# Kernel tuning notes

Hardware: AMD Instinct MI355X
Metric: run time of the kernel (lower is better)

The kernel has to match this reference:

```python
import jax, jax.numpy as jnp
import numpy as np

HIDDEN = 2048
N_HEADS = 32
N_KV = 8
HEAD_DIM = 128
EPS = 1e-6
THETA = 10000.0
WINDOW = 512
T = 2048


def _rms_norm(x, w, eps=EPS):
    # x: [..., d]
    var = jnp.mean(x * x, axis=-1, keepdims=True)
    return x * jax.lax.rsqrt(var + eps) * w


def _rope(x, positions):
    # neox-style full rotary, x: [T, H, d]
    d = x.shape[-1]
    inv_freq = 1.0 / (THETA ** (jnp.arange(0, d, 2, dtype=jnp.float32) / d))  # [d/2]
    ang = positions.astype(jnp.float32)[:, None] * inv_freq  # [T, d/2]
    cos = jnp.cos(ang)[:, None, :]  # [T,1,d/2]
    sin = jnp.sin(ang)[:, None, :]
    x1, x2 = x[..., : d // 2], x[..., d // 2 :]
    return jnp.concatenate([x1 * cos - x2 * sin, x2 * cos + x1 * sin], axis=-1)


def setup_inputs() -> dict:
    key = jax.random.key(0)
    ks = jax.random.split(key, 6)
    q_size = N_HEADS * HEAD_DIM
    kv_size = N_KV * HEAD_DIM
    s = 1.0 / np.sqrt(HIDDEN)
    return {
        "positions": jnp.arange(T, dtype=jnp.int32),
        "hidden_states": jax.random.normal(ks[0], (T, HIDDEN), dtype=jnp.float32),
        "w_qkv": jax.random.normal(ks[1], (HIDDEN, q_size + 2 * kv_size), dtype=jnp.float32) * s,
        "w_o": jax.random.normal(ks[2], (q_size, HIDDEN), dtype=jnp.float32) * s,
        "w_g": jax.random.normal(ks[3], (HIDDEN, N_HEADS), dtype=jnp.float32) * s,
        "q_norm_w": jnp.ones((HEAD_DIM,), dtype=jnp.float32),
        "k_norm_w": jnp.ones((HEAD_DIM,), dtype=jnp.float32),
    }


def reference(positions, hidden_states, w_qkv, w_o, w_g, q_norm_w, k_norm_w):
    t = hidden_states.shape[0]
    q_size = N_HEADS * HEAD_DIM
    kv_size = N_KV * HEAD_DIM
    scale = HEAD_DIM ** -0.5
    group = N_HEADS // N_KV

    qkv = hidden_states @ w_qkv  # [T, q+2kv]
    q = qkv[:, :q_size].reshape(t, N_HEADS, HEAD_DIM)
    k = qkv[:, q_size : q_size + kv_size].reshape(t, N_KV, HEAD_DIM)
    v = qkv[:, q_size + kv_size :].reshape(t, N_KV, HEAD_DIM)

    # per-head RMSNorm then RoPE
    q = _rope(_rms_norm(q, q_norm_w), positions)
    k = _rope(_rms_norm(k, k_norm_w), positions)

    # sliding-window causal attention with GQA (group queries per kv head)
    qg = q.reshape(t, N_KV, group, HEAD_DIM)
    scores = jnp.einsum("tkgd,skd->kgts", qg, k) * scale  # [Hkv,G,T,T]
    diff = positions[:, None] - positions[None, :]  # i - j
    mask = (diff >= 0) & (diff < WINDOW)  # causal + sliding window
    scores = jnp.where(mask[None, None], scores, -jnp.inf)
    probs = jax.nn.softmax(scores, axis=-1)
    attn = jnp.einsum("kgts,skd->tkgd", probs, v).reshape(t, N_HEADS, HEAD_DIM)

    # softplus gate per head, then output projection
    gate = jax.nn.softplus((hidden_states @ w_g).astype(jnp.float32)).astype(attn.dtype)
    attn = attn * gate[:, :, None]
    return attn.reshape(t, q_size) @ w_o
```

## Files before the change

### kernel.cpp

```cpp
#include <hip/hip_runtime.h>

typedef __attribute__((ext_vector_type(4))) float floatx4;
typedef __attribute__((ext_vector_type(8))) _Float16 half8;
typedef __attribute__((ext_vector_type(4))) _Float16 half4;

#define TT 2048
#define HIDDEN 2048
#define NH 32
#define NKV 8
#define HD 128
#define QSIZE 4096
#define KVSIZE 1024
#define QKVN 6144
#define QKVNP 6272
#define VOFF 5120
#define GOFF 6144
#define WINDOW 512

__global__ __launch_bounds__(256) void prep_kernel(
    const float* __restrict__ w_qkv, const float* __restrict__ w_o,
    const float* __restrict__ hidden, const float* __restrict__ w_g,
    _Float16* __restrict__ Wqkvt, _Float16* __restrict__ Wot,
    _Float16* __restrict__ Xb) {
  __shared__ float tile[64][68];
  int bid = blockIdx.x;
  int tid = threadIdx.x;
  if (bid >= 5120) {
    if (bid < 7168) {
      int i = ((bid - 5120) * 256 + tid) * 8;
      float4 a = *(const float4*)&hidden[i];
      float4 b = *(const float4*)&hidden[i + 4];
      alignas(16) _Float16 o[8] = {(_Float16)a.x, (_Float16)a.y, (_Float16)a.z, (_Float16)a.w,
                                   (_Float16)b.x, (_Float16)b.y, (_Float16)b.z, (_Float16)b.w};
      *(uint4*)&Xb[i] = *(const uint4*)o;
    } else if (bid < 7264) {
      int i = ((bid - 7168) * 256 + tid) * 8;
      *(uint4*)&Wqkvt[(size_t)(GOFF + NH) * HIDDEN + i] = (uint4){0, 0, 0, 0};
    } else {
      int br = (bid - 7264) * 32;
      int c = tid & 31, r0 = tid >> 5;
      __shared__ float gt[32][33];
#pragma unroll
      for (int i = 0; i < 4; ++i) {
        int r = r0 + 8 * i;
        gt[r][c] = w_g[(size_t)(br + r) * NH + c];
      }
      __syncthreads();
#pragma unroll
      for (int i = 0; i < 4; ++i) {
        int r = r0 + 8 * i;
        Wqkvt[(size_t)(GOFF + r) * HIDDEN + br + c] = (_Float16)gt[c][r];
      }
    }
    return;
  }
  const float* in;
  _Float16* out;
  int R, C, tilesX, t;
  if (bid < 3072) { in = w_qkv; out = Wqkvt; R = HIDDEN; C = QKVN; tilesX = 96; t = bid; }
  else           { in = w_o;   out = Wot;   R = QSIZE;  C = HIDDEN; tilesX = 32; t = bid - 3072; }
  int bc = (t % tilesX) * 64, br = (t / tilesX) * 64;
  int rr = tid >> 4, l16 = tid & 15;
#pragma unroll
  for (int it = 0; it < 4; ++it) {
    int r = rr + it * 16;
    *(float4*)&tile[r][l16 * 4] = *(const float4*)&in[(size_t)(br + r) * C + bc + l16 * 4];
  }
  __syncthreads();
  int orow = tid >> 2, rr0 = (tid & 3) * 16;
  alignas(16) _Float16 tmp[16];
#pragma unroll
  for (int jj = 0; jj < 16; ++jj) tmp[jj] = (_Float16)tile[rr0 + jj][orow];
  *(uint4*)&out[(size_t)(bc + orow) * R + br + rr0] = *(const uint4*)&tmp[0];
  *(uint4*)&out[(size_t)(bc + orow) * R + br + rr0 + 8] = *(const uint4*)&tmp[8];
}

__global__ __launch_bounds__(256) void repack_kv_kernel(const _Float16* __restrict__ Kh,
                                                        const _Float16* __restrict__ QKVh,
                                                        _Float16* __restrict__ Kf,
                                                        _Float16* __restrict__ Vf) {
  __shared__ _Float16 tile[64][136];
  int st = blockIdx.x, kh = blockIdx.y;
  int s0 = st * 64;
  if (blockIdx.z == 0) {
    _Float16* dst = Kf + (size_t)(kh * 32 + st) * 8192;
#pragma unroll
    for (int i = 0; i < 4; ++i) {
      int c = threadIdx.x + i * 256;
      int jt = c >> 8, kc = (c >> 6) & 3, quad = (c >> 4) & 3, n16 = c & 15;
      uint4 v = *(const uint4*)&Kh[((size_t)(s0 + jt * 16 + n16) * NKV + kh) * HD +
                                   kc * 32 + quad * 8];
      *(uint4*)&dst[c * 8] = v;
    }
  } else {
#pragma unroll
    for (int i = 0; i < 4; ++i) {
      int c = threadIdx.x + i * 256;
      int row = c >> 4, part = c & 15;
      *(uint4*)&tile[row][part * 8] =
          *(const uint4*)&QKVh[(size_t)(s0 + row) * QKVNP + VOFF + kh * HD + part * 8];
    }
    __syncthreads();
    _Float16* dst = Vf + (size_t)(kh * 32 + st) * 8192;
#pragma unroll
    for (int i = 0; i < 4; ++i) {
      int c = threadIdx.x + i * 256;
      int jd = c >> 7, kc = (c >> 6) & 1, quad = (c >> 4) & 3, n16 = c & 15;
      int d = jd * 16 + n16, sb = kc * 32 + quad * 8;
      alignas(16) _Float16 tmp[8];
#pragma unroll
      for (int j = 0; j < 8; ++j) tmp[j] = tile[sb + j][d];
      *(uint4*)&dst[c * 8] = *(const uint4*)tmp;
    }
  }
}

__device__ __forceinline__ void async16(const _Float16* g, _Float16* l) {
  __builtin_amdgcn_global_load_lds((const __attribute__((address_space(1))) void*)g,
                                   (__attribute__((address_space(3))) void*)l, 16, 0, 0);
}

__device__ __forceinline__ void swizzle_mn(int& m0, int& n0) {
  int ntiles = gridDim.y;
  int pid = blockIdx.x + blockIdx.y * gridDim.x;
  int band = pid / (8 * ntiles);
  int wi = pid - band * (8 * ntiles);
  m0 = (band * 8 + (wi & 7)) * 128;
  n0 = (wi >> 3) * 128;
}

template <typename OutT>
__global__ __launch_bounds__(256, 2) void gemm_bt_kernel(
    const _Float16* __restrict__ A, const _Float16* __restrict__ Bt,
    OutT* __restrict__ C, int M, int N, int K) {
  __shared__ _Float16 As[128 * 64];
  __shared__ _Float16 Bs[128 * 64];
  int tid = threadIdx.x;
  int wave = tid >> 6, lane = tid & 63;
  int wm = wave >> 1, wn = wave & 1;
  int m0, n0;
  swizzle_mn(m0, n0);
  int lr = lane & 15;
  int quad = lane >> 4;
  floatx4 acc[4][4];
#pragma unroll
  for (int i = 0; i < 4; ++i)
#pragma unroll
    for (int j = 0; j < 4; ++j) acc[i][j] = (floatx4){0.f, 0.f, 0.f, 0.f};

  for (int k0 = 0; k0 < K; k0 += 64) {
    __syncthreads();
#pragma unroll
    for (int it = 0; it < 4; ++it) {
      int c = tid + it * 256;
      int row = c >> 3, j = c & 7;
      int jj = j ^ (row & 7);
      _Float16* la = &As[it * 2048 + wave * 512];
      _Float16* lb = &Bs[it * 2048 + wave * 512];
      async16(&A[(size_t)(m0 + row) * K + k0 + jj * 8], la);
      async16(&Bt[(size_t)(n0 + row) * K + k0 + jj * 8], lb);
    }
    __syncthreads();
#pragma unroll
    for (int kc = 0; kc < 2; ++kc) {
      int ch = kc * 4 + quad;
      half8 a[4], b[4];
#pragma unroll
      for (int i = 0; i < 4; ++i) {
        int r = wm * 64 + i * 16 + lr;
        a[i] = *(const half8*)&As[r * 64 + (ch ^ (r & 7)) * 8];
      }
#pragma unroll
      for (int j = 0; j < 4; ++j) {
        int r = wn * 64 + j * 16 + lr;
        b[j] = *(const half8*)&Bs[r * 64 + (ch ^ (r & 7)) * 8];
      }
#pragma unroll
      for (int i = 0; i < 4; ++i)
#pragma unroll
        for (int j = 0; j < 4; ++j)
          acc[i][j] = __builtin_amdgcn_mfma_f32_16x16x32_f16(a[i], b[j], acc[i][j], 0, 0, 0);
    }
  }
  int rq = quad * 4;
#pragma unroll
  for (int i = 0; i < 4; ++i)
#pragma unroll
    for (int j = 0; j < 4; ++j)
#pragma unroll
      for (int r = 0; r < 4; ++r) {
        int row = m0 + wm * 64 + i * 16 + rq + r;
        int col = n0 + wn * 64 + j * 16 + lr;
        C[(size_t)row * N + col] = (OutT)acc[i][j][r];
      }
}

__global__ __launch_bounds__(256, 2) void gemm_bt_splitk_kernel(
    const _Float16* __restrict__ A, const _Float16* __restrict__ Bt,
    float* __restrict__ Cp, int M, int N, int K, int Ks) {
  __shared__ _Float16 As[128 * 64];
  __shared__ _Float16 Bs[128 * 64];
  int tid = threadIdx.x;
  int wave = tid >> 6, lane = tid & 63;
  int wm = wave >> 1, wn = wave & 1;
  int m0, n0;
  swizzle_mn(m0, n0);
  int kb = blockIdx.z * Ks;
  float* C = Cp + (size_t)blockIdx.z * M * N;
  int lr = lane & 15;
  int quad = lane >> 4;
  floatx4 acc[4][4];
#pragma unroll
  for (int i = 0; i < 4; ++i)
#pragma unroll
    for (int j = 0; j < 4; ++j) acc[i][j] = (floatx4){0.f, 0.f, 0.f, 0.f};

  for (int k0 = kb; k0 < kb + Ks; k0 += 64) {
    __syncthreads();
#pragma unroll
    for (int it = 0; it < 4; ++it) {
      int c = tid + it * 256;
      int row = c >> 3, j = c & 7;
      int jj = j ^ (row & 7);
      _Float16* la = &As[it * 2048 + wave * 512];
      _Float16* lb = &Bs[it * 2048 + wave * 512];
      async16(&A[(size_t)(m0 + row) * K + k0 + jj * 8], la);
      async16(&Bt[(size_t)(n0 + row) * K + k0 + jj * 8], lb);
    }
    __syncthreads();
#pragma unroll
    for (int kc = 0; kc < 2; ++kc) {
      int ch = kc * 4 + quad;
      half8 a[4], b[4];
#pragma unroll
      for (int i = 0; i < 4; ++i) {
        int r = wm * 64 + i * 16 + lr;
        a[i] = *(const half8*)&As[r * 64 + (ch ^ (r & 7)) * 8];
      }
#pragma unroll
      for (int j = 0; j < 4; ++j) {
        int r = wn * 64 + j * 16 + lr;
        b[j] = *(const half8*)&Bs[r * 64 + (ch ^ (r & 7)) * 8];
      }
#pragma unroll
      for (int i = 0; i < 4; ++i)
#pragma unroll
        for (int j = 0; j < 4; ++j)
          acc[i][j] = __builtin_amdgcn_mfma_f32_16x16x32_f16(a[i], b[j], acc[i][j], 0, 0, 0);
    }
  }
  int rq = quad * 4;
#pragma unroll
  for (int i = 0; i < 4; ++i)
#pragma unroll
    for (int j = 0; j < 4; ++j)
#pragma unroll
      for (int r = 0; r < 4; ++r) {
        int row = m0 + wm * 64 + i * 16 + rq + r;
        int col = n0 + wn * 64 + j * 16 + lr;
        C[(size_t)row * N + col] = acc[i][j][r];
      }
}

__global__ __launch_bounds__(256) void reduce2_kernel(const float* __restrict__ P,
                                                      float* __restrict__ out) {
  size_t i = ((size_t)blockIdx.x * 256 + threadIdx.x) * 8;
  const float* Q = P + (size_t)TT * HIDDEN;
  float4 a0 = *(const float4*)&P[i];
  float4 a1 = *(const float4*)&P[i + 4];
  float4 b0 = *(const float4*)&Q[i];
  float4 b1 = *(const float4*)&Q[i + 4];
  a0.x += b0.x; a0.y += b0.y; a0.z += b0.z; a0.w += b0.w;
  a1.x += b1.x; a1.y += b1.y; a1.z += b1.z; a1.w += b1.w;
  *(float4*)&out[i] = a0;
  *(float4*)&out[i + 4] = a1;
}

__global__ __launch_bounds__(256) void normrope_kernel(
    const _Float16* __restrict__ qkv, const float* __restrict__ qw,
    const float* __restrict__ kw, const int* __restrict__ positions,
    _Float16* __restrict__ qh, _Float16* __restrict__ khb) {
  int wid = blockIdx.x * 4 + (threadIdx.x >> 6);
  int lane = threadIdx.x & 63;
  int t, hh;
  const _Float16* src;
  _Float16* dst;
  const float* w;
  if (wid < TT * NH) {
    t = wid >> 5; hh = wid & 31;
    src = qkv + (size_t)t * QKVNP + hh * HD;
    dst = qh + ((size_t)t * NH + hh) * HD;
    w = qw;
  } else {
    int r = wid - TT * NH;
    t = r >> 3; hh = r & 7;
    src = qkv + (size_t)t * QKVNP + QSIZE + hh * HD;
    dst = khb + ((size_t)t * NKV + hh) * HD;
    w = kw;
  }
  float x1 = (float)src[lane];
  float x2 = (float)src[lane + 64];
  float ss = x1 * x1 + x2 * x2;
#pragma unroll
  for (int off = 1; off < 64; off <<= 1) ss += __shfl_xor(ss, off);
  float rr = rsqrtf(ss * (1.0f / 128.0f) + 1e-6f);
  float n1 = x1 * rr * w[lane];
  float n2 = x2 * rr * w[lane + 64];
  float pos = (float)positions[t];
  float invf = exp2f(-(float)lane * (13.287712379549449f / 64.0f));
  float ang = pos * invf;
  float sn, cs;
  sincosf(ang, &sn, &cs);
  dst[lane] = (_Float16)(n1 * cs - n2 * sn);
  dst[lane + 64] = (_Float16)(n2 * cs + n1 * sn);
}

#define PSTR 68
#define M0 8.0f
__global__ __launch_bounds__(256, 2) void attn_kernel(
    const _Float16* __restrict__ Qh, const _Float16* __restrict__ Kf,
    const _Float16* __restrict__ Vf, const _Float16* __restrict__ QKVh,
    _Float16* __restrict__ Og) {
  const float scale = 0.08838834764831845f;
  __shared__ _Float16 Ps[4][16 * PSTR];
  int tid = threadIdx.x;
  int wave = tid >> 6, lane = tid & 63;
  int n16 = lane & 15, quad = lane >> 4;
  int t0 = blockIdx.x * 16;
  int kh = blockIdx.y;
  int h = kh * 4 + wave;
  _Float16* ps = Ps[wave];

  half8 qf[4];
#pragma unroll
  for (int kc = 0; kc < 4; ++kc)
    qf[kc] = *(const half8*)&Qh[((size_t)(t0 + n16) * NH + h) * HD + kc * 32 + quad * 8];

  floatx4 O[8];
  float lp[4];
#pragma unroll
  for (int jd = 0; jd < 8; ++jd) O[jd] = (floatx4){0.f, 0.f, 0.f, 0.f};
#pragma unroll
  for (int r = 0; r < 4; ++r) lp[r] = 0.f;

  int lo = t0 - (WINDOW - 1);
  if (lo < 0) lo = 0;
  int st0 = lo >> 6;
  int st1 = t0 >> 6;

  half8 kfr[4][4];
  {
    const _Float16* kb = Kf + (size_t)(kh * 32 + st0) * 8192;
#pragma unroll
    for (int jt = 0; jt < 4; ++jt)
#pragma unroll
      for (int kc = 0; kc < 4; ++kc)
        kfr[jt][kc] = *(const half8*)&kb[(jt * 4 + kc) * 512 + lane * 8];
  }

  for (int st = st0; st <= st1; ++st) {
    int s0 = st * 64;
    const _Float16* vb = Vf + (size_t)(kh * 32 + st) * 8192;
    floatx4 S[4];
#pragma unroll
    for (int jt = 0; jt < 4; ++jt) S[jt] = (floatx4){0.f, 0.f, 0.f, 0.f};
#pragma unroll
    for (int jt = 0; jt < 4; ++jt)
#pragma unroll
      for (int kc = 0; kc < 4; ++kc)
        S[jt] = __builtin_amdgcn_mfma_f32_16x16x32_f16(qf[kc], kfr[jt][kc], S[jt], 0, 0, 0);
    if (st < st1) {
      const _Float16* kb = Kf + (size_t)(kh * 32 + st + 1) * 8192;
#pragma unroll
      for (int jt = 0; jt < 4; ++jt)
#pragma unroll
        for (int kc = 0; kc < 4; ++kc)
          kfr[jt][kc] = *(const half8*)&kb[(jt * 4 + kc) * 512 + lane * 8];
    }
    bool interior = (t0 >= s0 + 63) && (t0 + 15 - s0 < WINDOW);
    if (interior) {
#pragma unroll
      for (int r = 0; r < 4; ++r) {
        float rs = 0.f;
#pragma unroll
        for (int jt = 0; jt < 4; ++jt) {
          float p = __expf(__builtin_fmaf(S[jt][r], scale, -M0));
          rs += p;
          ps[(quad * 4 + r) * PSTR + jt * 16 + n16] = (_Float16)p;
        }
        lp[r] += rs;
      }
    } else {
#pragma unroll
      for (int r = 0; r < 4; ++r) {
        int tq = t0 + quad * 4 + r;
        float rs = 0.f;
#pragma unroll
        for (int jt = 0; jt < 4; ++jt) {
          int diff = tq - (s0 + jt * 16 + n16);
          bool ok = (diff >= 0) && (diff < WINDOW);
          float p = ok ? __expf(__builtin_fmaf(S[jt][r], scale, -M0)) : 0.f;
          rs += p;
          ps[(quad * 4 + r) * PSTR + jt * 16 + n16] = (_Float16)p;
        }
        lp[r] += rs;
      }
    }
    half8 pf[2];
#pragma unroll
    for (int kc = 0; kc < 2; ++kc) {
      half4 lo4 = *(const half4*)&ps[n16 * PSTR + kc * 32 + quad * 8];
      half4 hi4 = *(const half4*)&ps[n16 * PSTR + kc * 32 + quad * 8 + 4];
      pf[kc] = (half8){lo4[0], lo4[1], lo4[2], lo4[3], hi4[0], hi4[1], hi4[2], hi4[3]};
    }
#pragma unroll
    for (int jd = 0; jd < 8; ++jd) {
#pragma unroll
      for (int kc = 0; kc < 2; ++kc) {
        half8 vfr = *(const half8*)&vb[(jd * 2 + kc) * 512 + lane * 8];
        O[jd] = __builtin_amdgcn_mfma_f32_16x16x32_f16(pf[kc], vfr, O[jd], 0, 0, 0);
      }
    }
  }
#pragma unroll
  for (int r = 0; r < 4; ++r) {
    float l = lp[r];
#pragma unroll
    for (int off = 1; off < 16; off <<= 1) l += __shfl_xor(l, off);
    int t = t0 + quad * 4 + r;
    float gl = (float)QKVh[(size_t)t * QKVNP + GOFF + h];
    float g = (gl > 0.f) ? gl + log1pf(__expf(-gl)) : log1pf(__expf(gl));
    float inv = g / l;
#pragma unroll
    for (int jd = 0; jd < 8; ++jd)
      Og[(size_t)t * QSIZE + h * HD + jd * 16 + n16] = (_Float16)(O[jd][r] * inv);
  }
}

extern "C" void kernel_launch(void* const* d_in, const int* in_sizes, int n_in,
                              void* d_out, int out_size, void* d_ws, size_t ws_size,
                              hipStream_t stream) {
  const int* positions = (const int*)d_in[0];
  const float* hidden = (const float*)d_in[1];
  const float* w_qkv = (const float*)d_in[2];
  const float* w_o = (const float*)d_in[3];
  const float* w_g = (const float*)d_in[4];
  const float* q_norm_w = (const float*)d_in[5];
  const float* k_norm_w = (const float*)d_in[6];
  float* out = (float*)d_out;

  char* ws = (char*)d_ws;
  size_t off = 0;
  auto alloc = [&](size_t bytes) {
    void* p = ws + off;
    off += (bytes + 255) & ~(size_t)255;
    return p;
  };
  _Float16* Xb = (_Float16*)alloc((size_t)TT * HIDDEN * 2);
  _Float16* Wqkvt = (_Float16*)alloc((size_t)QKVNP * HIDDEN * 2);
  _Float16* Wot = (_Float16*)alloc((size_t)HIDDEN * QSIZE * 2);
  _Float16* QKVh = (_Float16*)alloc((size_t)TT * QKVNP * 2);
  _Float16* Qh = (_Float16*)alloc((size_t)TT * NH * HD * 2);
  _Float16* Kh = (_Float16*)alloc((size_t)TT * NKV * HD * 2);
  _Float16* Kf = (_Float16*)alloc((size_t)NKV * 32 * 8192 * 2);
  _Float16* Vf = (_Float16*)alloc((size_t)NKV * 32 * 8192 * 2);
  _Float16* Og = (_Float16*)alloc((size_t)TT * QSIZE * 2);
  float* Cp = (float*)ws;

  prep_kernel<<<7328, 256, 0, stream>>>(w_qkv, w_o, hidden, w_g, Wqkvt, Wot, Xb);
  gemm_bt_kernel<_Float16><<<dim3(TT / 128, QKVNP / 128), 256, 0, stream>>>(
      Xb, Wqkvt, QKVh, TT, QKVNP, HIDDEN);
  normrope_kernel<<<(TT * (NH + NKV)) / 4, 256, 0, stream>>>(QKVh, q_norm_w, k_norm_w,
                                                             positions, Qh, Kh);
  repack_kv_kernel<<<dim3(32, NKV, 2), 256, 0, stream>>>(Kh, QKVh, Kf, Vf);
  attn_kernel<<<dim3(TT / 16, NKV), 256, 0, stream>>>(Qh, Kf, Vf, QKVh, Og);
  gemm_bt_splitk_kernel<<<dim3(TT / 128, HIDDEN / 128, 2), 256, 0, stream>>>(
      Og, Wot, Cp, TT, HIDDEN, QSIZE, QSIZE / 2);
  reduce2_kernel<<<(TT * HIDDEN) / (256 * 8), 256, 0, stream>>>(Cp, out);
}
```

Measured before the change: 335.9 us.

## Replace QKV GEMM with 256x256-tile 8-wave kernel using pipelined async LDS loads

The QKV projection GEMM moves from a 128x128-tile, 4-wave kernel to a 256x256-tile, 512-thread kernel. The new kernel double-buffers K-slices in 128KB of LDS and interleaves the async global-to-LDS loads of the next slice with MFMA quarters, using explicit vmcnt waits, barriers and setprio. The weight buffer is padded to 6400 rows so N divides by 256, and the extra rows are zero-filled in prep. The aim is more data reuse per tile and overlap of loads with compute; the cost is a smaller grid (8x25 blocks), which may leave CUs underused, plus wasted padded columns.

```diff
diff --git a/kernel.cpp b/kernel.cpp
--- a/kernel.cpp
+++ b/kernel.cpp
@@ -13,6 +13,7 @@
 #define KVSIZE 1024
 #define QKVN 6144
 #define QKVNP 6272
+#define WQR 6400
 #define VOFF 5120
 #define GOFF 6144
 #define WINDOW 512
@@ -33,11 +34,11 @@
       alignas(16) _Float16 o[8] = {(_Float16)a.x, (_Float16)a.y, (_Float16)a.z, (_Float16)a.w,
                                    (_Float16)b.x, (_Float16)b.y, (_Float16)b.z, (_Float16)b.w};
       *(uint4*)&Xb[i] = *(const uint4*)o;
-    } else if (bid < 7264) {
+    } else if (bid < 7392) {
       int i = ((bid - 7168) * 256 + tid) * 8;
       *(uint4*)&Wqkvt[(size_t)(GOFF + NH) * HIDDEN + i] = (uint4){0, 0, 0, 0};
     } else {
-      int br = (bid - 7264) * 32;
+      int br = (bid - 7392) * 32;
       int c = tid & 31, r0 = tid >> 5;
       __shared__ float gt[32][33];
 #pragma unroll
@@ -120,6 +121,134 @@
                                    (__attribute__((address_space(3))) void*)l, 16, 0, 0);
 }
 
+#define G256_K 2048
+
+#define STG_A(ob, mh, kt)                                                        \
+  async16(As0 + (size_t)(mh) * 64 * G256_K + (kt), &lds[(ob) + ((mh) * 64 + r0A0) * 64]); \
+  async16(As1 + (size_t)(mh) * 64 * G256_K + (kt), &lds[(ob) + ((mh) * 64 + r0A1) * 64]);
+#define STG_B(ob, nh, kt)                                                        \
+  async16(Bs0 + (size_t)(nh) * 32 * G256_K + (kt), &lds[(ob) + 16384 + ((nh) * 32 + r0B0) * 64]); \
+  async16(Bs1 + (size_t)(nh) * 32 * G256_K + (kt), &lds[(ob) + 16384 + ((nh) * 32 + r0B1) * 64]);
+
+#define LD_A(mh)                                                                 \
+  _Pragma("unroll") for (int fm = 0; fm < 4; ++fm)                               \
+  _Pragma("unroll") for (int ks = 0; ks < 2; ++ks)                               \
+    aA[fm][ks] = *(const half8*)&LA[(wm * 128 + (mh) * 64 + fm * 16 + lr) * 64 + \
+                                    (((ks * 4 + quad) ^ l7) * 8)];
+#define LD_B(DST, nh)                                                            \
+  _Pragma("unroll") for (int fn = 0; fn < 2; ++fn)                               \
+  _Pragma("unroll") for (int ks = 0; ks < 2; ++ks)                               \
+    DST[fn][ks] = *(const half8*)&LB[(wn * 64 + (nh) * 32 + fn * 16 + lr) * 64 + \
+                                     (((ks * 4 + quad) ^ l7) * 8)];
+#define MFMAQ(BS, mh, nh)                                                        \
+  __builtin_amdgcn_s_setprio(1);                                                 \
+  _Pragma("unroll") for (int fm = 0; fm < 4; ++fm)                               \
+  _Pragma("unroll") for (int fn = 0; fn < 2; ++fn)                               \
+  _Pragma("unroll") for (int ks = 0; ks < 2; ++ks)                               \
+    acc[(mh) * 4 + fm][(nh) * 2 + fn] = __builtin_amdgcn_mfma_f32_16x16x32_f16(  \
+        aA[fm][ks], BS[fn][ks], acc[(mh) * 4 + fm][(nh) * 2 + fn], 0, 0, 0);     \
+  __builtin_amdgcn_s_setprio(0);
+#define VMW4 asm volatile("s_waitcnt vmcnt(4)" ::: "memory")
+#define VMW2 asm volatile("s_waitcnt vmcnt(2)" ::: "memory")
+#define VMW0 asm volatile("s_waitcnt vmcnt(0)" ::: "memory")
+#define BAR __builtin_amdgcn_s_barrier()
+#define SB0 __builtin_amdgcn_sched_barrier(0)
+
+__global__ __launch_bounds__(512, 2) void gemm256_kernel(
+    const _Float16* __restrict__ A, const _Float16* __restrict__ Bt,
+    _Float16* __restrict__ C) {
+  __shared__ _Float16 lds[65536];
+  int tid = threadIdx.x;
+  int wave = tid >> 6, lane = tid & 63;
+  int wm = wave >> 2, wn = wave & 3;
+  int lr = lane & 15, quad = lane >> 4, l7 = lane & 7, l3 = lane >> 3;
+  int m0 = blockIdx.x * 256, n0 = blockIdx.y * 256;
+
+  int q0 = wave * 2, q1 = q0 + 1;
+  int r0A0 = (q0 >> 3) * 128 + (q0 & 7) * 8;
+  int r0A1 = (q1 >> 3) * 128 + (q1 & 7) * 8;
+  int r0B0 = (q0 >> 2) * 64 + (q0 & 3) * 8;
+  int r0B1 = (q1 >> 2) * 64 + (q1 & 3) * 8;
+  int gA8 = (l7 ^ l3) * 8;
+
+  const _Float16* As0 = A + (size_t)(m0 + r0A0 + l3) * G256_K + gA8;
+  const _Float16* As1 = A + (size_t)(m0 + r0A1 + l3) * G256_K + gA8;
+  const _Float16* Bs0 = Bt + (size_t)(n0 + r0B0 + l3) * G256_K + gA8;
+  const _Float16* Bs1 = Bt + (size_t)(n0 + r0B1 + l3) * G256_K + gA8;
+
+  floatx4 acc[8][4];
+#pragma unroll
+  for (int i = 0; i < 8; ++i)
+#pragma unroll
+    for (int j = 0; j < 4; ++j) acc[i][j] = (floatx4){0.f, 0.f, 0.f, 0.f};
+
+  STG_A(0, 0, 0);
+  STG_B(0, 0, 0);
+  STG_B(0, 1, 0);
+  STG_A(0, 1, 0);
+  VMW4;
+  BAR;
+  SB0;
+
+  half8 aA[4][2], b0[2][2], b1[2][2];
+
+  for (int t = 0; t < 32; ++t) {
+    int bb = (t & 1) << 15;
+    int ob = bb ^ 32768;
+    int ktn = (t + 1) * 64;
+    bool stg = (t < 31);
+    const _Float16* LA = &lds[bb];
+    const _Float16* LB = &lds[bb + 16384];
+
+    LD_A(0);
+    LD_B(b0, 0);
+    if (stg) { STG_A(ob, 0, ktn); }
+    BAR;
+    MFMAQ(b0, 0, 0);
+    if (stg) VMW4; else VMW2;
+    BAR;
+    SB0;
+
+    LD_B(b1, 1);
+    if (stg) { STG_B(ob, 0, ktn); }
+    BAR;
+    MFMAQ(b1, 0, 1);
+    if (stg) VMW4; else VMW0;
+    BAR;
+    SB0;
+
+    LD_A(1);
+    if (stg) { STG_B(ob, 1, ktn); }
+    BAR;
+    MFMAQ(b0, 1, 0);
+    BAR;
+    SB0;
+
+    if (stg) { STG_A(ob, 1, ktn); }
+    BAR;
+    MFMAQ(b1, 1, 1);
+    if (stg) VMW4;
+    BAR;
+    SB0;
+  }
+
+#pragma unroll
+  for (int mh = 0; mh < 2; ++mh)
+#pragma unroll
+    for (int fm = 0; fm < 4; ++fm)
+#pragma unroll
+      for (int nh = 0; nh < 2; ++nh)
+#pragma unroll
+        for (int fn = 0; fn < 2; ++fn)
+#pragma unroll
+          for (int rr = 0; rr < 4; ++rr) {
+            int row = m0 + wm * 128 + mh * 64 + fm * 16 + quad * 4 + rr;
+            int col = n0 + wn * 64 + nh * 32 + fn * 16 + lr;
+            if (col < QKVNP)
+              C[(size_t)row * QKVNP + col] = (_Float16)acc[mh * 4 + fm][nh * 2 + fn][rr];
+          }
+}
+
 __device__ __forceinline__ void swizzle_mn(int& m0, int& n0) {
   int ntiles = gridDim.y;
   int pid = blockIdx.x + blockIdx.y * gridDim.x;
@@ -127,72 +256,6 @@
   int wi = pid - band * (8 * ntiles);
   m0 = (band * 8 + (wi & 7)) * 128;
   n0 = (wi >> 3) * 128;
-}
-
-template <typename OutT>
-__global__ __launch_bounds__(256, 2) void gemm_bt_kernel(
-    const _Float16* __restrict__ A, const _Float16* __restrict__ Bt,
-    OutT* __restrict__ C, int M, int N, int K) {
-  __shared__ _Float16 As[128 * 64];
-  __shared__ _Float16 Bs[128 * 64];
-  int tid = threadIdx.x;
-  int wave = tid >> 6, lane = tid & 63;
-  int wm = wave >> 1, wn = wave & 1;
-  int m0, n0;
-  swizzle_mn(m0, n0);
-  int lr = lane & 15;
-  int quad = lane >> 4;
-  floatx4 acc[4][4];
-#pragma unroll
-  for (int i = 0; i < 4; ++i)
-#pragma unroll
-    for (int j = 0; j < 4; ++j) acc[i][j] = (floatx4){0.f, 0.f, 0.f, 0.f};
-
-  for (int k0 = 0; k0 < K; k0 += 64) {
-    __syncthreads();
-#pragma unroll
-    for (int it = 0; it < 4; ++it) {
-      int c = tid + it * 256;
-      int row = c >> 3, j = c & 7;
-      int jj = j ^ (row & 7);
-      _Float16* la = &As[it * 2048 + wave * 512];
-      _Float16* lb = &Bs[it * 2048 + wave * 512];
-      async16(&A[(size_t)(m0 + row) * K + k0 + jj * 8], la);
-      async16(&Bt[(size_t)(n0 + row) * K + k0 + jj * 8], lb);
-    }
-    __syncthreads();
-#pragma unroll
-    for (int kc = 0; kc < 2; ++kc) {
-      int ch = kc * 4 + quad;
-      half8 a[4], b[4];
-#pragma unroll
-      for (int i = 0; i < 4; ++i) {
-        int r = wm * 64 + i * 16 + lr;
-        a[i] = *(const half8*)&As[r * 64 + (ch ^ (r & 7)) * 8];
-      }
-#pragma unroll
-      for (int j = 0; j < 4; ++j) {
-        int r = wn * 64 + j * 16 + lr;
-        b[j] = *(const half8*)&Bs[r * 64 + (ch ^ (r & 7)) * 8];
-      }
-#pragma unroll
-      for (int i = 0; i < 4; ++i)
-#pragma unroll
-        for (int j = 0; j < 4; ++j)
-          acc[i][j] = __builtin_amdgcn_mfma_f32_16x16x32_f16(a[i], b[j], acc[i][j], 0, 0, 0);
-    }
-  }
-  int rq = quad * 4;
-#pragma unroll
-  for (int i = 0; i < 4; ++i)
-#pragma unroll
-    for (int j = 0; j < 4; ++j)
-#pragma unroll
-      for (int r = 0; r < 4; ++r) {
-        int row = m0 + wm * 64 + i * 16 + rq + r;
-        int col = n0 + wn * 64 + j * 16 + lr;
-        C[(size_t)row * N + col] = (OutT)acc[i][j][r];
-      }
 }
 
 __global__ __launch_bounds__(256, 2) void gemm_bt_splitk_kernel(
@@ -457,7 +520,7 @@
     return p;
   };
   _Float16* Xb = (_Float16*)alloc((size_t)TT * HIDDEN * 2);
-  _Float16* Wqkvt = (_Float16*)alloc((size_t)QKVNP * HIDDEN * 2);
+  _Float16* Wqkvt = (_Float16*)alloc((size_t)WQR * HIDDEN * 2);
   _Float16* Wot = (_Float16*)alloc((size_t)HIDDEN * QSIZE * 2);
   _Float16* QKVh = (_Float16*)alloc((size_t)TT * QKVNP * 2);
   _Float16* Qh = (_Float16*)alloc((size_t)TT * NH * HD * 2);
@@ -467,9 +530,8 @@
   _Float16* Og = (_Float16*)alloc((size_t)TT * QSIZE * 2);
   float* Cp = (float*)ws;
 
-  prep_kernel<<<7328, 256, 0, stream>>>(w_qkv, w_o, hidden, w_g, Wqkvt, Wot, Xb);
-  gemm_bt_kernel<_Float16><<<dim3(TT / 128, QKVNP / 128), 256, 0, stream>>>(
-      Xb, Wqkvt, QKVh, TT, QKVNP, HIDDEN);
+  prep_kernel<<<7456, 256, 0, stream>>>(w_qkv, w_o, hidden, w_g, Wqkvt, Wot, Xb);
+  gemm256_kernel<<<dim3(TT / 256, WQR / 256), 512, 0, stream>>>(Xb, Wqkvt, QKVh);
   normrope_kernel<<<(TT * (NH + NKV)) / 4, 256, 0, stream>>>(QKVh, q_norm_w, k_norm_w,
                                                              positions, Qh, Kh);
   repack_kv_kernel<<<dim3(32, NKV, 2), 256, 0, stream>>>(Kh, QKVh, Kf, Vf);
```

After: 315.6 us. -6.1%, faster.

## Replace QKV GEMM with 256x256-tile, 4-stage async-pipelined kernel

Applied to the files above, without the earlier changes.

Replaces the 128x128-tile QKV projection GEMM with a 512-thread kernel that uses 256x256 output tiles, a four-buffer async global-to-LDS pipeline with explicit vmcnt waits and raw barriers, and MFMA priority bumps. Larger tiles raise arithmetic intensity and the deeper pipeline overlaps loads with compute. The weight buffer is padded to 6400 rows and zero-filled so that the 25 column tiles need no K-side guards, with stores masked to the real column count. The grid is remapped to 200 blocks, and the 128 KB of LDS per block limits occupancy.

```diff
diff --git a/kernel.cpp b/kernel.cpp
--- a/kernel.cpp
+++ b/kernel.cpp
@@ -13,6 +13,7 @@
 #define KVSIZE 1024
 #define QKVN 6144
 #define QKVNP 6272
+#define WQR 6400
 #define VOFF 5120
 #define GOFF 6144
 #define WINDOW 512
@@ -33,11 +34,11 @@
       alignas(16) _Float16 o[8] = {(_Float16)a.x, (_Float16)a.y, (_Float16)a.z, (_Float16)a.w,
                                    (_Float16)b.x, (_Float16)b.y, (_Float16)b.z, (_Float16)b.w};
       *(uint4*)&Xb[i] = *(const uint4*)o;
-    } else if (bid < 7264) {
+    } else if (bid < 7392) {
       int i = ((bid - 7168) * 256 + tid) * 8;
       *(uint4*)&Wqkvt[(size_t)(GOFF + NH) * HIDDEN + i] = (uint4){0, 0, 0, 0};
     } else {
-      int br = (bid - 7264) * 32;
+      int br = (bid - 7392) * 32;
       int c = tid & 31, r0 = tid >> 5;
       __shared__ float gt[32][33];
 #pragma unroll
@@ -120,6 +121,98 @@
                                    (__attribute__((address_space(3))) void*)l, 16, 0, 0);
 }
 
+#define G256_K 2048
+
+#define STG32(tt)                                                                \
+  { int bb_ = ((tt) & 3) * 16384; int ko_ = (tt) * 32;                           \
+    async16(As0 + ko_, &lds[bb_ + wave * 1024]);                                 \
+    async16(As1 + ko_, &lds[bb_ + wave * 1024 + 512]);                           \
+    async16(Bs0 + ko_, &lds[bb_ + 8192 + wave * 1024]);                          \
+    async16(Bs1 + ko_, &lds[bb_ + 8192 + wave * 1024 + 512]); }
+
+#define GEMM_BODY(tt)                                                            \
+  { const _Float16* LA = &lds[((tt) & 3) * 16384];                               \
+    const _Float16* LB = LA + 8192;                                              \
+    half8 a[8], b[4];                                                            \
+    _Pragma("unroll") for (int i = 0; i < 8; ++i)                                \
+      a[i] = *(const half8*)&LA[(wm * 128 + i * 16 + lr) * 32 + swz];            \
+    _Pragma("unroll") for (int j = 0; j < 4; ++j)                                \
+      b[j] = *(const half8*)&LB[(wn * 64 + j * 16 + lr) * 32 + swz];             \
+    __builtin_amdgcn_s_setprio(1);                                               \
+    _Pragma("unroll") for (int i = 0; i < 8; ++i)                                \
+    _Pragma("unroll") for (int j = 0; j < 4; ++j)                                \
+      acc[i][j] = __builtin_amdgcn_mfma_f32_16x16x32_f16(a[i], b[j], acc[i][j], 0, 0, 0); \
+    __builtin_amdgcn_s_setprio(0); }
+
+#define VMW(n) asm volatile("s_waitcnt vmcnt(" #n ")" ::: "memory")
+#define BAR __builtin_amdgcn_s_barrier()
+#define SB0 __builtin_amdgcn_sched_barrier(0)
+
+__global__ __launch_bounds__(512, 2) void gemm256_kernel(
+    const _Float16* __restrict__ A, const _Float16* __restrict__ Bt,
+    _Float16* __restrict__ C) {
+  __shared__ _Float16 lds[65536];
+  int tid = threadIdx.x;
+  int wave = tid >> 6, lane = tid & 63;
+  int wm = wave >> 2, wn = wave & 3;
+  int lr = lane & 15, quad = lane >> 4;
+  int swz = (quad ^ (lr & 3)) * 8;
+
+  int bid = blockIdx.x;
+  int o = (bid & 7) * 25 + (bid >> 3);
+  int m0 = (o & 7) * 256, n0 = (o >> 3) * 256;
+
+  int lrow = lane >> 2;
+  int sslot = ((lane & 3) ^ (lrow & 3)) * 8;
+  int crA0 = wave * 32, crA1 = wave * 32 + 16;
+  const _Float16* As0 = A + (size_t)(m0 + crA0 + lrow) * G256_K + sslot;
+  const _Float16* As1 = A + (size_t)(m0 + crA1 + lrow) * G256_K + sslot;
+  const _Float16* Bs0 = Bt + (size_t)(n0 + crA0 + lrow) * G256_K + sslot;
+  const _Float16* Bs1 = Bt + (size_t)(n0 + crA1 + lrow) * G256_K + sslot;
+
+  floatx4 acc[8][4];
+#pragma unroll
+  for (int i = 0; i < 8; ++i)
+#pragma unroll
+    for (int j = 0; j < 4; ++j) acc[i][j] = (floatx4){0.f, 0.f, 0.f, 0.f};
+
+  STG32(0);
+  STG32(1);
+  STG32(2);
+  VMW(8);
+  BAR;
+  SB0;
+
+  for (int t = 0; t < 61; ++t) {
+    STG32(t + 3);
+    GEMM_BODY(t);
+    VMW(8);
+    BAR;
+    SB0;
+  }
+  GEMM_BODY(61);
+  VMW(4);
+  BAR;
+  SB0;
+  GEMM_BODY(62);
+  VMW(0);
+  BAR;
+  SB0;
+  GEMM_BODY(63);
+
+#pragma unroll
+  for (int i = 0; i < 8; ++i)
+#pragma unroll
+    for (int j = 0; j < 4; ++j)
+#pragma unroll
+      for (int rr = 0; rr < 4; ++rr) {
+        int row = m0 + wm * 128 + i * 16 + quad * 4 + rr;
+        int col = n0 + wn * 64 + j * 16 + lr;
+        if (col < QKVNP)
+          C[(size_t)row * QKVNP + col] = (_Float16)acc[i][j][rr];
+      }
+}
+
 __device__ __forceinline__ void swizzle_mn(int& m0, int& n0) {
   int ntiles = gridDim.y;
   int pid = blockIdx.x + blockIdx.y * gridDim.x;
@@ -127,72 +220,6 @@
   int wi = pid - band * (8 * ntiles);
   m0 = (band * 8 + (wi & 7)) * 128;
   n0 = (wi >> 3) * 128;
-}
-
-template <typename OutT>
-__global__ __launch_bounds__(256, 2) void gemm_bt_kernel(
-    const _Float16* __restrict__ A, const _Float16* __restrict__ Bt,
-    OutT* __restrict__ C, int M, int N, int K) {
-  __shared__ _Float16 As[128 * 64];
-  __shared__ _Float16 Bs[128 * 64];
-  int tid = threadIdx.x;
-  int wave = tid >> 6, lane = tid & 63;
-  int wm = wave >> 1, wn = wave & 1;
-  int m0, n0;
-  swizzle_mn(m0, n0);
-  int lr = lane & 15;
-  int quad = lane >> 4;
-  floatx4 acc[4][4];
-#pragma unroll
-  for (int i = 0; i < 4; ++i)
-#pragma unroll
-    for (int j = 0; j < 4; ++j) acc[i][j] = (floatx4){0.f, 0.f, 0.f, 0.f};
-
-  for (int k0 = 0; k0 < K; k0 += 64) {
-    __syncthreads();
-#pragma unroll
-    for (int it = 0; it < 4; ++it) {
-      int c = tid + it * 256;
-      int row = c >> 3, j = c & 7;
-      int jj = j ^ (row & 7);
-      _Float16* la = &As[it * 2048 + wave * 512];
-      _Float16* lb = &Bs[it * 2048 + wave * 512];
-      async16(&A[(size_t)(m0 + row) * K + k0 + jj * 8], la);
-      async16(&Bt[(size_t)(n0 + row) * K + k0 + jj * 8], lb);
-    }
-    __syncthreads();
-#pragma unroll
-    for (int kc = 0; kc < 2; ++kc) {
-      int ch = kc * 4 + quad;
-      half8 a[4], b[4];
-#pragma unroll
-      for (int i = 0; i < 4; ++i) {
-        int r = wm * 64 + i * 16 + lr;
-        a[i] = *(const half8*)&As[r * 64 + (ch ^ (r & 7)) * 8];
-      }
-#pragma unroll
-      for (int j = 0; j < 4; ++j) {
-        int r = wn * 64 + j * 16 + lr;
-        b[j] = *(const half8*)&Bs[r * 64 + (ch ^ (r & 7)) * 8];
-      }
-#pragma unroll
-      for (int i = 0; i < 4; ++i)
-#pragma unroll
-        for (int j = 0; j < 4; ++j)
-          acc[i][j] = __builtin_amdgcn_mfma_f32_16x16x32_f16(a[i], b[j], acc[i][j], 0, 0, 0);
-    }
-  }
-  int rq = quad * 4;
-#pragma unroll
-  for (int i = 0; i < 4; ++i)
-#pragma unroll
-    for (int j = 0; j < 4; ++j)
-#pragma unroll
-      for (int r = 0; r < 4; ++r) {
-        int row = m0 + wm * 64 + i * 16 + rq + r;
-        int col = n0 + wn * 64 + j * 16 + lr;
-        C[(size_t)row * N + col] = (OutT)acc[i][j][r];
-      }
 }
 
 __global__ __launch_bounds__(256, 2) void gemm_bt_splitk_kernel(
@@ -457,7 +484,7 @@
     return p;
   };
   _Float16* Xb = (_Float16*)alloc((size_t)TT * HIDDEN * 2);
-  _Float16* Wqkvt = (_Float16*)alloc((size_t)QKVNP * HIDDEN * 2);
+  _Float16* Wqkvt = (_Float16*)alloc((size_t)WQR * HIDDEN * 2);
   _Float16* Wot = (_Float16*)alloc((size_t)HIDDEN * QSIZE * 2);
   _Float16* QKVh = (_Float16*)alloc((size_t)TT * QKVNP * 2);
   _Float16* Qh = (_Float16*)alloc((size_t)TT * NH * HD * 2);
@@ -467,9 +494,8 @@
   _Float16* Og = (_Float16*)alloc((size_t)TT * QSIZE * 2);
   float* Cp = (float*)ws;
 
-  prep_kernel<<<7328, 256, 0, stream>>>(w_qkv, w_o, hidden, w_g, Wqkvt, Wot, Xb);
-  gemm_bt_kernel<_Float16><<<dim3(TT / 128, QKVNP / 128), 256, 0, stream>>>(
-      Xb, Wqkvt, QKVh, TT, QKVNP, HIDDEN);
+  prep_kernel<<<7456, 256, 0, stream>>>(w_qkv, w_o, hidden, w_g, Wqkvt, Wot, Xb);
+  gemm256_kernel<<<200, 512, 0, stream>>>(Xb, Wqkvt, QKVh);
   normrope_kernel<<<(TT * (NH + NKV)) / 4, 256, 0, stream>>>(QKVh, q_norm_w, k_norm_w,
                                                              positions, Qh, Kh);
   repack_kv_kernel<<<dim3(32, NKV, 2), 256, 0, stream>>>(Kh, QKVh, Kf, Vf);
```

Result: faster. 320.6 us (-4.6%).
